# Kernel optimization log

Hardware: AMD Instinct MI355X
Metric: run time of the kernel (lower is better)

Reference implementation:

```python
import jax, jax.numpy as jnp
import numpy as np

B_ROWS = 262144
D = 64            # features
N_UNMASKED = D // 2
HID = 128
N_BINS = 8
BOUND = 3.0
MIN_BIN_W = 1e-3
MIN_BIN_H = 1e-3
MIN_DERIV = 1e-3
LN_EPS = 1e-6


def setup_inputs() -> dict:
    key = jax.random.key(0)
    ks = jax.random.split(key, 8)
    x = jax.random.normal(ks[0], (B_ROWS, D), dtype=jnp.float32)
    # conditioner MLP params (lecun-normal-ish)
    W0 = jax.random.normal(ks[1], (N_UNMASKED, HID), dtype=jnp.float32) / np.sqrt(N_UNMASKED)
    b0 = jnp.zeros((HID,), jnp.float32)
    g0 = jnp.ones((HID,), jnp.float32)
    be0 = jnp.zeros((HID,), jnp.float32)
    W1 = jax.random.normal(ks[2], (HID, HID), dtype=jnp.float32) / np.sqrt(HID)
    b1 = jnp.zeros((HID,), jnp.float32)
    g1 = jnp.ones((HID,), jnp.float32)
    be1 = jnp.zeros((HID,), jnp.float32)
    # spline output projection: HID -> N_UNMASKED * (3*K + 1)
    n_out = N_UNMASKED * (3 * N_BINS + 1)
    Wp = jax.random.normal(ks[3], (HID, n_out), dtype=jnp.float32) / np.sqrt(HID)
    bp = jnp.zeros((n_out,), jnp.float32)
    return {"x": x, "W0": W0, "b0": b0, "g0": g0, "be0": be0,
            "W1": W1, "b1": b1, "g1": g1, "be1": be1, "Wp": Wp, "bp": bp}


def _layer_norm(h, scale, bias):
    mu = jnp.mean(h, axis=-1, keepdims=True)
    var = jnp.mean(jnp.square(h - mu), axis=-1, keepdims=True)
    return (h - mu) * jax.lax.rsqrt(var + LN_EPS) * scale + bias


def _rqs_forward(xu, widths, heights, derivs):
    """Monotone rational-quadratic spline (Durkan et al. 2019), forward.
    xu: (..., D2); widths/heights: (..., D2, K); derivs: (..., D2, K+1)."""
    K = widths.shape[-1]
    cw = jnp.concatenate([jnp.zeros_like(widths[..., :1]), jnp.cumsum(widths, -1)], -1) - BOUND
    ch = jnp.concatenate([jnp.zeros_like(heights[..., :1]), jnp.cumsum(heights, -1)], -1) - BOUND
    inside = (xu > -BOUND) & (xu < BOUND)
    xc = jnp.clip(xu, -BOUND, BOUND)
    # bin search: index of bin containing xc
    idx = jnp.clip(jnp.sum(xc[..., None] >= cw, axis=-1) - 1, 0, K - 1)
    g = lambda t, i: jnp.take_along_axis(t, i[..., None], axis=-1)[..., 0]
    w_k = g(widths, idx); x_k = g(cw, idx)
    h_k = g(heights, idx); y_k = g(ch, idx)
    d_k = g(derivs, idx); d_k1 = g(derivs, idx + 1)
    s = h_k / w_k                       # bin slope
    theta = (xc - x_k) / w_k
    t1m = theta * (1.0 - theta)
    den = s + (d_k1 + d_k - 2.0 * s) * t1m
    y_in = y_k + h_k * (s * theta * theta + d_k * t1m) / den
    ld_in = (2.0 * jnp.log(s)
             + jnp.log(d_k1 * theta * theta + 2.0 * s * t1m + d_k * (1.0 - theta) ** 2)
             - 2.0 * jnp.log(den))
    y = jnp.where(inside, y_in, xu)           # identity outside domain
    ld = jnp.where(inside, ld_in, 0.0)
    return y, jnp.sum(ld, axis=-1)


def _forward(x, W0, b0, g0, be0, W1, b1, g1, be1, Wp, bp):
    # split by mask parity 0: even idx masked, odd idx transformed
    xm = x[..., 0::2]
    xu = x[..., 1::2]
    # conditioner MLP (LayerNorm + relu, residual when widths match)
    h1 = jax.nn.relu(_layer_norm(xm @ W0 + b0, g0, be0))
    h2 = jax.nn.relu(_layer_norm(h1 @ W1 + b1, g1, be1)) + h1  # residual (128==128)
    raw = (h2 @ Wp + bp).reshape(x.shape[:-1] + (N_UNMASKED, 3 * N_BINS + 1))
    # unconstrained -> rqs params
    w_raw = raw[..., :N_BINS]
    h_raw = raw[..., N_BINS:2 * N_BINS]
    d_raw = raw[..., 2 * N_BINS:]
    widths = jax.nn.softmax(w_raw, axis=-1)
    widths = (MIN_BIN_W + (1.0 - MIN_BIN_W * N_BINS) * widths) * (2.0 * BOUND)
    heights = jax.nn.softmax(h_raw, axis=-1)
    heights = (MIN_BIN_H + (1.0 - MIN_BIN_H * N_BINS) * heights) * (2.0 * BOUND)
    derivs = jax.nn.softplus(d_raw) + MIN_DERIV
    yu, log_det = _rqs_forward(xu, widths, heights, derivs)
    # merge by mask
    y = jnp.zeros_like(x)
    y = y.at[..., 0::2].set(xm)
    y = y.at[..., 1::2].set(yu)
    return y, log_det


def reference(x, W0, b0, g0, be0, W1, b1, g1, be1, Wp, bp):
    return _forward(x, W0, b0, g0, be0, W1, b1, g1, be1, Wp, bp)
```

## Files before the change

kernel.cpp:

```cpp
#include <hip/hip_runtime.h>
#include <hip/hip_bf16.h>
#include <stdint.h>

#define NROWS 262144

typedef __bf16 bf16x8 __attribute__((ext_vector_type(8)));
typedef float f32x4 __attribute__((ext_vector_type(4)));
typedef float f32x16 __attribute__((ext_vector_type(16)));

#define MFMA16(a,b,c) __builtin_amdgcn_mfma_f32_16x16x32_bf16(a,b,c,0,0,0)
#define MFMA32(a,b,c) __builtin_amdgcn_mfma_f32_32x32x16_bf16(a,b,c,0,0,0)

#define WS_WP 0
#define WS_W1 524288
#define WS_W0 589824
#define WS_BP 606208

#define RS0 0
#define RS1 16384
#define XMA 32768
#define W0L 40960
#define YUL 32768
#define LDL 49152
#define XUL 57344

__device__ __forceinline__ unsigned short f2bf(float f){
    unsigned int u = __float_as_uint(f);
    u = (u + 0x7FFFu + ((u >> 16) & 1u)) >> 16;
    return (unsigned short)u;
}
__device__ __forceinline__ float bf2f(unsigned short h){
    return __uint_as_float(((unsigned int)h) << 16);
}

__global__ __launch_bounds__(256) void prep_kernel(
    const float* __restrict__ W0, const float* __restrict__ W1,
    const float* __restrict__ Wp, const float* __restrict__ bp,
    char* __restrict__ ws)
{
    int tid = blockIdx.x * 256 + threadIdx.x;
    if (tid < 32768){
        int d = tid >> 10, r = tid & 1023;
        int plane = r >> 9, oct = (r >> 5) & 15, p = r & 31;
        unsigned short cell[8];
        #pragma unroll
        for (int j = 0; j < 8; j++){
            int k = oct*8 + j;
            float v = (p < 25) ? Wp[k*800 + d*25 + p] : 0.f;
            unsigned short hi = f2bf(v);
            cell[j] = plane ? f2bf(v - bf2f(hi)) : hi;
        }
        *(uint4*)(ws + WS_WP + d*16384 + plane*8192 + oct*512 + p*16) = *(uint4*)cell;
    } else if (tid < 36864){
        int i = tid - 32768;
        int kr = i >> 10, r = i & 1023;
        int plane = r >> 9, q = (r >> 7) & 3, n = r & 127;
        unsigned short cell[8];
        #pragma unroll
        for (int j = 0; j < 8; j++){
            int k = kr*32 + q*8 + j;
            float v = W1[k*128 + n];
            unsigned short hi = f2bf(v);
            cell[j] = plane ? f2bf(v - bf2f(hi)) : hi;
        }
        *(uint4*)(ws + WS_W1 + kr*16384 + plane*8192 + (q*128+n)*16) = *(uint4*)cell;
    } else if (tid < 37888){
        int i = tid - 36864;
        int plane = i >> 9, g = (i >> 7) & 3, n = i & 127;
        unsigned short cell[8];
        #pragma unroll
        for (int j = 0; j < 8; j++){
            int k = g*8 + j;
            float v = W0[k*128 + n];
            unsigned short hi = f2bf(v);
            cell[j] = plane ? f2bf(v - bf2f(hi)) : hi;
        }
        *(uint4*)(ws + WS_W0 + plane*8192 + (g*128+n)*16) = *(uint4*)cell;
    } else if (tid < 38912){
        int i = tid - 37888;
        int d = i >> 5, n = i & 31;
        ((float*)(ws + WS_BP))[i] = (n < 25) ? bp[d*25 + n] : 0.f;
    }
}

__global__ __launch_bounds__(256, 2) void main_kernel(
    const float* __restrict__ x,
    const float* __restrict__ pb0, const float* __restrict__ pg0, const float* __restrict__ pbe0,
    const float* __restrict__ pb1, const float* __restrict__ pg1, const float* __restrict__ pbe1,
    const char* __restrict__ ws,
    float* __restrict__ yout, float* __restrict__ ldout)
{
    __shared__ __align__(16) char smem[65536];
    const int t = threadIdx.x;
    const int r0 = blockIdx.x * 64;
    const int w = t >> 6, lane = t & 63, l16 = lane & 15, q = lane >> 4;
    const f32x4 fzero = {0.f, 0.f, 0.f, 0.f};

    auto stage16k = [&](int dstoff, int srcoff){
        #pragma unroll
        for (int k = 0; k < 4; k++){
            int cell = t + 256*k;
            ((uint4*)(smem + dstoff))[cell] = ((const uint4*)(ws + srcoff))[cell];
        }
    };

    #pragma unroll
    for (int k = 0; k < 4; k++){
        int i = t + 256*k;
        int row = i >> 4, s = i & 15;
        float4 v = ((const float4*)(x + (size_t)(r0 + row) * 64))[s];
        unsigned short h0 = f2bf(v.x), h1s = f2bf(v.z);
        unsigned short l0 = f2bf(v.x - bf2f(h0)), l1 = f2bf(v.z - bf2f(h1s));
        int g = s >> 2, ofs = (s & 3) * 4;
        *(unsigned int*)(smem + XMA + (g*64 + row)*16 + ofs) = (unsigned int)h0 | ((unsigned int)h1s << 16);
        *(unsigned int*)(smem + XMA + 4096 + (g*64 + row)*16 + ofs) = (unsigned int)l0 | ((unsigned int)l1 << 16);
        *(float*)(smem + XUL + ((2*s)*64 + row)*4) = v.y;
        *(float*)(smem + XUL + ((2*s+1)*64 + row)*4) = v.w;
    }
    stage16k(W0L, WS_W0);
    stage16k(RS0, WS_W1);
    __syncthreads();

    float h1r[8][4];
    {
        bf16x8 a_h = *(const bf16x8*)(smem + XMA + (q*64 + 16*w + l16)*16);
        bf16x8 a_l = *(const bf16x8*)(smem + XMA + 4096 + (q*64 + 16*w + l16)*16);
        f32x4 c0[8];
        #pragma unroll
        for (int nt = 0; nt < 8; nt++){
            int n = nt*16 + l16;
            bf16x8 b_h = *(const bf16x8*)(smem + W0L + (q*128 + n)*16);
            bf16x8 b_l = *(const bf16x8*)(smem + W0L + 8192 + (q*128 + n)*16);
            f32x4 acc = fzero;
            acc = MFMA16(a_h, b_l, acc);
            acc = MFMA16(a_l, b_h, acc);
            acc = MFMA16(a_h, b_h, acc);
            c0[nt] = acc;
        }
        float s1[4] = {0,0,0,0}, s2[4] = {0,0,0,0};
        #pragma unroll
        for (int nt = 0; nt < 8; nt++){
            float bv = pb0[nt*16 + l16];
            #pragma unroll
            for (int rg = 0; rg < 4; rg++){
                float v = c0[nt][rg] + bv;
                c0[nt][rg] = v; s1[rg] += v; s2[rg] += v*v;
            }
        }
        #pragma unroll
        for (int m = 1; m < 16; m <<= 1)
            #pragma unroll
            for (int rg = 0; rg < 4; rg++){
                s1[rg] += __shfl_xor(s1[rg], m, 64);
                s2[rg] += __shfl_xor(s2[rg], m, 64);
            }
        #pragma unroll
        for (int rg = 0; rg < 4; rg++){
            float mean = s1[rg] * 0.0078125f;
            float var  = s2[rg] * 0.0078125f - mean*mean;
            s1[rg] = mean; s2[rg] = rsqrtf(var + 1e-6f);
        }
        #pragma unroll
        for (int nt = 0; nt < 8; nt++){
            float gv = pg0[nt*16 + l16], bev = pbe0[nt*16 + l16];
            #pragma unroll
            for (int rg = 0; rg < 4; rg++){
                float hv = (c0[nt][rg] - s1[rg]) * s2[rg] * gv + bev;
                h1r[nt][rg] = fmaxf(hv, 0.f);
            }
        }
    }
    __syncthreads();

    stage16k(RS1, WS_W1 + 16384);
    bf16x8 ah1[4], al1[4];
    {
        char* sb = smem + 32768 + w*4096;
        #pragma unroll
        for (int nt = 0; nt < 8; nt++){
            int col = nt*16 + l16;
            #pragma unroll
            for (int rg = 0; rg < 4; rg++)
                *(unsigned short*)(sb + ((col>>3)*16 + q*4+rg)*16 + (col&7)*2) = f2bf(h1r[nt][rg]);
        }
        #pragma unroll
        for (int kr = 0; kr < 4; kr++)
            ah1[kr] = *(const bf16x8*)(sb + ((kr*4+q)*16 + l16)*16);
        #pragma unroll
        for (int nt = 0; nt < 8; nt++){
            int col = nt*16 + l16;
            #pragma unroll
            for (int rg = 0; rg < 4; rg++){
                unsigned short hi = f2bf(h1r[nt][rg]);
                *(unsigned short*)(sb + ((col>>3)*16 + q*4+rg)*16 + (col&7)*2) = f2bf(h1r[nt][rg] - bf2f(hi));
            }
        }
        #pragma unroll
        for (int kr = 0; kr < 4; kr++)
            al1[kr] = *(const bf16x8*)(sb + ((kr*4+q)*16 + l16)*16);
    }

    f32x4 c1[8];
    #pragma unroll
    for (int nt = 0; nt < 8; nt++) c1[nt] = fzero;
    auto g1round = [&](int base, bf16x8 ah, bf16x8 al){
        #pragma unroll
        for (int nt = 0; nt < 8; nt++){
            int n = nt*16 + l16;
            bf16x8 bhv = *(const bf16x8*)(smem + base + (q*128 + n)*16);
            bf16x8 blv = *(const bf16x8*)(smem + base + 8192 + (q*128 + n)*16);
            c1[nt] = MFMA16(ah, blv, c1[nt]);
            c1[nt] = MFMA16(al, bhv, c1[nt]);
            c1[nt] = MFMA16(ah, bhv, c1[nt]);
        }
    };
    g1round(RS0, ah1[0], al1[0]);
    __syncthreads();
    stage16k(RS0, WS_W1 + 32768);
    g1round(RS1, ah1[1], al1[1]);
    __syncthreads();
    stage16k(RS1, WS_W1 + 49152);
    g1round(RS0, ah1[2], al1[2]);
    __syncthreads();
    g1round(RS1, ah1[3], al1[3]);

    {
        float s1[4] = {0,0,0,0}, s2[4] = {0,0,0,0};
        #pragma unroll
        for (int nt = 0; nt < 8; nt++){
            float bv = pb1[nt*16 + l16];
            #pragma unroll
            for (int rg = 0; rg < 4; rg++){
                float v = c1[nt][rg] + bv;
                c1[nt][rg] = v; s1[rg] += v; s2[rg] += v*v;
            }
        }
        #pragma unroll
        for (int m = 1; m < 16; m <<= 1)
            #pragma unroll
            for (int rg = 0; rg < 4; rg++){
                s1[rg] += __shfl_xor(s1[rg], m, 64);
                s2[rg] += __shfl_xor(s2[rg], m, 64);
            }
        #pragma unroll
        for (int rg = 0; rg < 4; rg++){
            float mean = s1[rg] * 0.0078125f;
            float var  = s2[rg] * 0.0078125f - mean*mean;
            s1[rg] = mean; s2[rg] = rsqrtf(var + 1e-6f);
        }
        #pragma unroll
        for (int nt = 0; nt < 8; nt++){
            float gv = pg1[nt*16 + l16], bev = pbe1[nt*16 + l16];
            #pragma unroll
            for (int rg = 0; rg < 4; rg++){
                float hv = (c1[nt][rg] - s1[rg]) * s2[rg] * gv + bev;
                h1r[nt][rg] = fmaxf(hv, 0.f) + h1r[nt][rg];
            }
        }
    }
    __syncthreads();

    #pragma unroll
    for (int nt = 0; nt < 8; nt++){
        int k = nt*16 + l16;
        #pragma unroll
        for (int rg = 0; rg < 4; rg++){
            int row = 16*w + q*4 + rg;
            float val = h1r[nt][rg];
            unsigned short hi = f2bf(val);
            int addr = row*256 + ((((k>>3) ^ (row&15)) & 15)*16) + (k&7)*2;
            *(unsigned short*)(smem + RS0 + addr) = hi;
            *(unsigned short*)(smem + RS1 + addr) = f2bf(val - bf2f(hi));
        }
    }
    __syncthreads();
    bf16x8 bh[2][8], bl[2][8];
    #pragma unroll
    for (int T = 0; T < 2; T++)
        #pragma unroll
        for (int kb = 0; kb < 8; kb++){
            int r = T*32 + (lane & 31);
            int oct = kb*2 + (lane >> 5);
            int addr = r*256 + (((oct ^ (r&15)) & 15)*16);
            bh[T][kb] = *(const bf16x8*)(smem + RS0 + addr);
            bl[T][kb] = *(const bf16x8*)(smem + RS1 + addr);
        }

    const char* wpl = ws + WS_WP + lane*16;
    const float* bpf = (const float*)(ws + WS_BP);
    float* xuLf = (float*)(smem + XUL);
    float* yuLf = (float*)(smem + YUL);
    const uint4 zero4 = {0,0,0,0};
    const bool pok = (lane & 31) < 25;
    const int hh = lane >> 5;
    const int d0 = w*8;
    uint4 A0[8], A1[8];
    #pragma unroll
    for (int kk = 0; kk < 8; kk++){ A0[kk] = zero4; A1[kk] = zero4; }
    if (pok){
        #pragma unroll
        for (int kk = 0; kk < 4; kk++){
            A0[kk]   = *(const uint4*)(wpl + d0*16384 + kk*1024);
            A0[4+kk] = *(const uint4*)(wpl + d0*16384 + 8192 + kk*1024);
        }
    }
    float ld_acc = 0.f;
    for (int i = 0; i < 8; i++){
        int c = d0 + i;
        if (pok){
            #pragma unroll
            for (int kk = 0; kk < 4; kk++){
                A1[kk]   = *(const uint4*)(wpl + c*16384 + (4+kk)*1024);
                A1[4+kk] = *(const uint4*)(wpl + c*16384 + 8192 + (4+kk)*1024);
            }
        }
        f32x16 t0, t1;
        #pragma unroll
        for (int z = 0; z < 16; z++){ t0[z] = 0.f; t1[z] = 0.f; }
        #pragma unroll
        for (int kk = 0; kk < 4; kk++){
            bf16x8 ahh = *(bf16x8*)&A0[kk];
            bf16x8 all = *(bf16x8*)&A0[4+kk];
            t0 = MFMA32(ahh, bl[0][kk], t0); t1 = MFMA32(ahh, bl[1][kk], t1);
            t0 = MFMA32(all, bh[0][kk], t0); t1 = MFMA32(all, bh[1][kk], t1);
            t0 = MFMA32(ahh, bh[0][kk], t0); t1 = MFMA32(ahh, bh[1][kk], t1);
        }
        if (i < 7 && pok){
            #pragma unroll
            for (int kk = 0; kk < 4; kk++){
                A0[kk]   = *(const uint4*)(wpl + (c+1)*16384 + kk*1024);
                A0[4+kk] = *(const uint4*)(wpl + (c+1)*16384 + 8192 + kk*1024);
            }
        }
        #pragma unroll
        for (int kk = 0; kk < 4; kk++){
            bf16x8 ahh = *(bf16x8*)&A1[kk];
            bf16x8 all = *(bf16x8*)&A1[4+kk];
            t0 = MFMA32(ahh, bl[0][4+kk], t0); t1 = MFMA32(ahh, bl[1][4+kk], t1);
            t0 = MFMA32(all, bh[0][4+kk], t0); t1 = MFMA32(all, bh[1][4+kk], t1);
            t0 = MFMA32(ahh, bh[0][4+kk], t0); t1 = MFMA32(ahh, bh[1][4+kk], t1);
        }
        float xu0 = xuLf[c*64 + (lane & 31)];
        float xu1 = xuLf[c*64 + 32 + (lane & 31)];
        float xc0 = fminf(fmaxf(xu0, -3.f), 3.f);
        float xc1 = fminf(fmaxf(xu1, -3.f), 3.f);
        float4 bq0 = *(const float4*)(bpf + c*32 + 0  + 4*hh);
        float4 bq1 = *(const float4*)(bpf + c*32 + 8  + 4*hh);
        float4 bq2 = *(const float4*)(bpf + c*32 + 16 + 4*hh);
        float  bq3 = bpf[c*32 + 24 + 4*hh];
        float wv0[4], wv1[4], hv0[4], hv1[4], dv0[4], dv1[4];
        #pragma unroll
        for (int jj = 0; jj < 4; jj++){
            wv0[jj] = t0[jj] + bq0[jj];  hv0[jj] = t0[4+jj] + bq1[jj];  dv0[jj] = t0[8+jj] + bq2[jj];
            wv1[jj] = t1[jj] + bq0[jj];  hv1[jj] = t1[4+jj] + bq1[jj];  dv1[jj] = t1[8+jj] + bq2[jj];
        }
        float dx0 = t0[12] + bq3, dx1 = t1[12] + bq3;
        float bd0 = __shfl_xor(hh ? dv0[0] : dx0, 32, 64);
        float bd1 = __shfl_xor(hh ? dv1[0] : dx1, 32, 64);
        auto softscale = [&](float* a){
            float m = fmaxf(fmaxf(a[0],a[1]), fmaxf(a[2],a[3]));
            m = fmaxf(m, __shfl_xor(m, 32, 64));
            float e0 = __expf(a[0]-m), e1 = __expf(a[1]-m), e2 = __expf(a[2]-m), e3 = __expf(a[3]-m);
            float s = (e0+e1)+(e2+e3);
            s += __shfl_xor(s, 32, 64);
            float sc = 5.952f / s;
            a[0] = fmaf(e0, sc, 0.006f); a[1] = fmaf(e1, sc, 0.006f);
            a[2] = fmaf(e2, sc, 0.006f); a[3] = fmaf(e3, sc, 0.006f);
        };
        softscale(wv0); softscale(hv0); softscale(wv1); softscale(hv1);
        auto candf = [&](float* wv, float* hv, float* dv, float bdr, float xc,
                         float& X, float& Y, float& W, float& H, float& DK, float& DK1, float& V){
            float pw0 = wv[0], pw1 = pw0+wv[1], pw2 = pw1+wv[2], pw3 = pw2+wv[3];
            float ph0 = hv[0], ph1 = ph0+hv[1], ph2 = ph1+hv[2], ph3 = ph2+hv[3];
            float offw = __shfl_xor(pw3, 32, 64);
            float offh = __shfl_xor(ph3, 32, 64);
            float bw = hh ? (offw - 3.f) : -3.f;
            float by = hh ? (offh - 3.f) : -3.f;
            X = bw; Y = by; W = wv[0]; H = hv[0]; DK = dv[0]; DK1 = dv[1];
            float e1_ = bw + pw0, e2_ = bw + pw1, e3_ = bw + pw2;
            if (xc >= e1_){ X = e1_; Y = by + ph0; W = wv[1]; H = hv[1]; DK = dv[1]; DK1 = dv[2]; }
            if (xc >= e2_){ X = e2_; Y = by + ph1; W = wv[2]; H = hv[2]; DK = dv[2]; DK1 = dv[3]; }
            if (xc >= e3_){ X = e3_; Y = by + ph2; W = wv[3]; H = hv[3]; DK = dv[3]; DK1 = bdr;  }
            V = (!hh || xc >= bw) ? 1.f : 0.f;
        };
        float X0,Y0,Wc0,Hc0,K0,K10,V0, X1,Y1,Wc1,Hc1,K1,K11,V1;
        candf(wv0, hv0, dv0, bd0, xc0, X0,Y0,Wc0,Hc0,K0,K10,V0);
        candf(wv1, hv1, dv1, bd1, xc1, X1,Y1,Wc1,Hc1,K1,K11,V1);
        float rX  = __shfl_xor(hh ? X0  : X1 , 32, 64);
        float rY  = __shfl_xor(hh ? Y0  : Y1 , 32, 64);
        float rW  = __shfl_xor(hh ? Wc0 : Wc1, 32, 64);
        float rH  = __shfl_xor(hh ? Hc0 : Hc1, 32, 64);
        float rK  = __shfl_xor(hh ? K0  : K1 , 32, 64);
        float rK1 = __shfl_xor(hh ? K10 : K11, 32, 64);
        float rV  = __shfl_xor(hh ? V0  : V1 , 32, 64);
        float oX  = hh ? X1  : X0,  oY  = hh ? Y1  : Y0,  oW = hh ? Wc1 : Wc0;
        float oH  = hh ? Hc1 : Hc0, oK  = hh ? K1  : K0,  oK1 = hh ? K11 : K10;
        float oV  = hh ? V1  : V0;
        bool useh1 = ((hh ? oV : rV) > 0.5f);
        bool useOwn = (hh != 0) == useh1;
        float X = useOwn ? oX : rX,  Y = useOwn ? oY : rY;
        float W = useOwn ? oW : rW,  H = useOwn ? oH : rH;
        float K = useOwn ? oK : rK,  K1s = useOwn ? oK1 : rK1;
        float xu = hh ? xu1 : xu0;
        float xc = hh ? xc1 : xc0;
        float DKs  = fmaxf(K, 0.f)   + __logf(1.f + __expf(-fabsf(K)))   + 0.001f;
        float DK1s = fmaxf(K1s, 0.f) + __logf(1.f + __expf(-fabsf(K1s))) + 0.001f;
        float iw = 1.f / W;
        float s_ = H * iw;
        float th = (xc - X) * iw;
        float om = 1.f - th;
        float t1m = th * om;
        float den = s_ + (DK1s + DKs - 2.f*s_) * t1m;
        float yin = Y + H * (s_*th*th + DKs*t1m) / den;
        float num2 = DK1s*th*th + 2.f*s_*t1m + DKs*om*om;
        float ldin = 2.f*__logf(s_) + __logf(num2) - 2.f*__logf(den);
        bool inside = (xu > -3.f) && (xu < 3.f);
        yuLf[c*64 + lane] = inside ? yin : xu;
        ld_acc += inside ? ldin : 0.f;
    }

    *(float*)(smem + LDL + (w*64 + lane)*4) = ld_acc;
    __syncthreads();
    if (t < 64){
        const float* lp = (const float*)(smem + LDL);
        ldout[r0 + t] = (lp[t] + lp[64 + t]) + (lp[128 + t] + lp[192 + t]);
    }
    {
        int row = t >> 2, part = t & 3;
        const float* xrow = x + (size_t)(r0 + row)*64;
        float* yrow = yout + (size_t)(r0 + row)*64;
        const float* yuL = (const float*)(smem + YUL);
        #pragma unroll
        for (int j = 0; j < 4; j++){
            int s = part*4 + j;
            float4 xv = ((const float4*)xrow)[s];
            float4 o;
            o.x = xv.x; o.z = xv.z;
            o.y = yuL[(2*s)*64 + row];
            o.w = yuL[(2*s+1)*64 + row];
            ((float4*)yrow)[s] = o;
        }
    }
}

extern "C" void kernel_launch(void* const* d_in, const int* in_sizes, int n_in,
                              void* d_out, int out_size, void* d_ws, size_t ws_size,
                              hipStream_t stream)
{
    const float* x   = (const float*)d_in[0];
    const float* W0  = (const float*)d_in[1];
    const float* b0  = (const float*)d_in[2];
    const float* g0  = (const float*)d_in[3];
    const float* be0 = (const float*)d_in[4];
    const float* W1  = (const float*)d_in[5];
    const float* b1  = (const float*)d_in[6];
    const float* g1  = (const float*)d_in[7];
    const float* be1 = (const float*)d_in[8];
    const float* Wp  = (const float*)d_in[9];
    const float* bp  = (const float*)d_in[10];
    float* y = (float*)d_out;
    float* ldo = y + (size_t)NROWS * 64;
    char* ws = (char*)d_ws;

    hipLaunchKernelGGL(prep_kernel, dim3(152), dim3(256), 0, stream, W0, W1, Wp, bp, ws);
    hipLaunchKernelGGL(main_kernel, dim3(4096), dim3(256), 0, stream,
                       x, b0, g0, be0, b1, g1, be1, ws, y, ldo);
}
```

Baseline: 410.5 us.

## Shrink LDS footprint to fit three blocks per CU

Reduces shared memory from 64 KB to 48 KB by loading W0 fragments directly into registers, staging W1 in two 16 KB halves, and reusing buffers for the yu/log-det outputs, then raises launch bounds to 3 blocks per SM. The projection B fragments are now read from LDS inside the loop instead of being held in 32 register vectors, freeing registers for the higher occupancy target. It costs extra LDS reads per chunk in the projection loop and an extra barrier, and the register cap at 3 waves/SIMD may cause spills.

```diff
diff --git a/kernel.cpp b/kernel.cpp
--- a/kernel.cpp
+++ b/kernel.cpp
@@ -16,13 +16,10 @@
 #define WS_W0 589824
 #define WS_BP 606208
 
-#define RS0 0
-#define RS1 16384
-#define XMA 32768
-#define W0L 40960
-#define YUL 32768
-#define LDL 49152
-#define XUL 57344
+#define W1A 0
+#define W1B 16384
+#define XM  32768
+#define XU  40960
 
 __device__ __forceinline__ unsigned short f2bf(float f){
     unsigned int u = __float_as_uint(f);
@@ -83,14 +80,14 @@
     }
 }
 
-__global__ __launch_bounds__(256, 2) void main_kernel(
+__global__ __launch_bounds__(256, 3) void main_kernel(
     const float* __restrict__ x,
     const float* __restrict__ pb0, const float* __restrict__ pg0, const float* __restrict__ pbe0,
     const float* __restrict__ pb1, const float* __restrict__ pg1, const float* __restrict__ pbe1,
     const char* __restrict__ ws,
     float* __restrict__ yout, float* __restrict__ ldout)
 {
-    __shared__ __align__(16) char smem[65536];
+    __shared__ __align__(16) char smem[49152];
     const int t = threadIdx.x;
     const int r0 = blockIdx.x * 64;
     const int w = t >> 6, lane = t & 63, l16 = lane & 15, q = lane >> 4;
@@ -104,6 +101,13 @@
         }
     };
 
+    uint4 w0h[8], w0l[8];
+    #pragma unroll
+    for (int nt = 0; nt < 8; nt++){
+        int n = nt*16 + l16;
+        w0h[nt] = *(const uint4*)(ws + WS_W0 + (q*128 + n)*16);
+        w0l[nt] = *(const uint4*)(ws + WS_W0 + 8192 + (q*128 + n)*16);
+    }
     #pragma unroll
     for (int k = 0; k < 4; k++){
         int i = t + 256*k;
@@ -112,25 +116,24 @@
         unsigned short h0 = f2bf(v.x), h1s = f2bf(v.z);
         unsigned short l0 = f2bf(v.x - bf2f(h0)), l1 = f2bf(v.z - bf2f(h1s));
         int g = s >> 2, ofs = (s & 3) * 4;
-        *(unsigned int*)(smem + XMA + (g*64 + row)*16 + ofs) = (unsigned int)h0 | ((unsigned int)h1s << 16);
-        *(unsigned int*)(smem + XMA + 4096 + (g*64 + row)*16 + ofs) = (unsigned int)l0 | ((unsigned int)l1 << 16);
-        *(float*)(smem + XUL + ((2*s)*64 + row)*4) = v.y;
-        *(float*)(smem + XUL + ((2*s+1)*64 + row)*4) = v.w;
-    }
-    stage16k(W0L, WS_W0);
-    stage16k(RS0, WS_W1);
+        *(unsigned int*)(smem + XM + (g*64 + row)*16 + ofs) = (unsigned int)h0 | ((unsigned int)h1s << 16);
+        *(unsigned int*)(smem + XM + 4096 + (g*64 + row)*16 + ofs) = (unsigned int)l0 | ((unsigned int)l1 << 16);
+        *(float*)(smem + XU + ((2*s)*64 + row)*4) = v.y;
+        *(float*)(smem + XU + ((2*s+1)*64 + row)*4) = v.w;
+    }
+    stage16k(W1A, WS_W1);
+    stage16k(W1B, WS_W1 + 16384);
     __syncthreads();
 
     float h1r[8][4];
     {
-        bf16x8 a_h = *(const bf16x8*)(smem + XMA + (q*64 + 16*w + l16)*16);
-        bf16x8 a_l = *(const bf16x8*)(smem + XMA + 4096 + (q*64 + 16*w + l16)*16);
+        bf16x8 a_h = *(const bf16x8*)(smem + XM + (q*64 + 16*w + l16)*16);
+        bf16x8 a_l = *(const bf16x8*)(smem + XM + 4096 + (q*64 + 16*w + l16)*16);
         f32x4 c0[8];
         #pragma unroll
         for (int nt = 0; nt < 8; nt++){
-            int n = nt*16 + l16;
-            bf16x8 b_h = *(const bf16x8*)(smem + W0L + (q*128 + n)*16);
-            bf16x8 b_l = *(const bf16x8*)(smem + W0L + 8192 + (q*128 + n)*16);
+            bf16x8 b_h = *(bf16x8*)&w0h[nt];
+            bf16x8 b_l = *(bf16x8*)&w0l[nt];
             f32x4 acc = fzero;
             acc = MFMA16(a_h, b_l, acc);
             acc = MFMA16(a_l, b_h, acc);
@@ -172,32 +175,39 @@
     }
     __syncthreads();
 
-    stage16k(RS1, WS_W1 + 16384);
     bf16x8 ah1[4], al1[4];
     {
-        char* sb = smem + 32768 + w*4096;
-        #pragma unroll
-        for (int nt = 0; nt < 8; nt++){
-            int col = nt*16 + l16;
-            #pragma unroll
-            for (int rg = 0; rg < 4; rg++)
-                *(unsigned short*)(sb + ((col>>3)*16 + q*4+rg)*16 + (col&7)*2) = f2bf(h1r[nt][rg]);
-        }
-        #pragma unroll
-        for (int kr = 0; kr < 4; kr++)
-            ah1[kr] = *(const bf16x8*)(sb + ((kr*4+q)*16 + l16)*16);
-        #pragma unroll
-        for (int nt = 0; nt < 8; nt++){
-            int col = nt*16 + l16;
-            #pragma unroll
-            for (int rg = 0; rg < 4; rg++){
-                unsigned short hi = f2bf(h1r[nt][rg]);
-                *(unsigned short*)(sb + ((col>>3)*16 + q*4+rg)*16 + (col&7)*2) = f2bf(h1r[nt][rg] - bf2f(hi));
-            }
-        }
-        #pragma unroll
-        for (int kr = 0; kr < 4; kr++)
-            al1[kr] = *(const bf16x8*)(sb + ((kr*4+q)*16 + l16)*16);
+        char* sb = smem + XM + w*2048;
+        #pragma unroll
+        for (int half = 0; half < 2; half++){
+            #pragma unroll
+            for (int nt = half*4; nt < half*4 + 4; nt++){
+                int col = nt*16 + l16;
+                int gg = (col >> 3) - half*8;
+                #pragma unroll
+                for (int rg = 0; rg < 4; rg++)
+                    *(unsigned short*)(sb + (gg*16 + q*4+rg)*16 + (col&7)*2) = f2bf(h1r[nt][rg]);
+            }
+            #pragma unroll
+            for (int kr = half*2; kr < half*2 + 2; kr++)
+                ah1[kr] = *(const bf16x8*)(sb + (((kr*4+q) - half*8)*16 + l16)*16);
+        }
+        #pragma unroll
+        for (int half = 0; half < 2; half++){
+            #pragma unroll
+            for (int nt = half*4; nt < half*4 + 4; nt++){
+                int col = nt*16 + l16;
+                int gg = (col >> 3) - half*8;
+                #pragma unroll
+                for (int rg = 0; rg < 4; rg++){
+                    unsigned short hi = f2bf(h1r[nt][rg]);
+                    *(unsigned short*)(sb + (gg*16 + q*4+rg)*16 + (col&7)*2) = f2bf(h1r[nt][rg] - bf2f(hi));
+                }
+            }
+            #pragma unroll
+            for (int kr = half*2; kr < half*2 + 2; kr++)
+                al1[kr] = *(const bf16x8*)(sb + (((kr*4+q) - half*8)*16 + l16)*16);
+        }
     }
 
     f32x4 c1[8];
@@ -214,15 +224,14 @@
             c1[nt] = MFMA16(ah, bhv, c1[nt]);
         }
     };
-    g1round(RS0, ah1[0], al1[0]);
-    __syncthreads();
-    stage16k(RS0, WS_W1 + 32768);
-    g1round(RS1, ah1[1], al1[1]);
-    __syncthreads();
-    stage16k(RS1, WS_W1 + 49152);
-    g1round(RS0, ah1[2], al1[2]);
-    __syncthreads();
-    g1round(RS1, ah1[3], al1[3]);
+    g1round(W1A, ah1[0], al1[0]);
+    g1round(W1B, ah1[1], al1[1]);
+    __syncthreads();
+    stage16k(W1A, WS_W1 + 32768);
+    stage16k(W1B, WS_W1 + 49152);
+    __syncthreads();
+    g1round(W1A, ah1[2], al1[2]);
+    g1round(W1B, ah1[3], al1[3]);
 
     {
         float s1[4] = {0,0,0,0}, s2[4] = {0,0,0,0};
@@ -269,31 +278,24 @@
             float val = h1r[nt][rg];
             unsigned short hi = f2bf(val);
             int addr = row*256 + ((((k>>3) ^ (row&15)) & 15)*16) + (k&7)*2;
-            *(unsigned short*)(smem + RS0 + addr) = hi;
-            *(unsigned short*)(smem + RS1 + addr) = f2bf(val - bf2f(hi));
-        }
-    }
-    __syncthreads();
-    bf16x8 bh[2][8], bl[2][8];
-    #pragma unroll
-    for (int T = 0; T < 2; T++)
-        #pragma unroll
-        for (int kb = 0; kb < 8; kb++){
-            int r = T*32 + (lane & 31);
-            int oct = kb*2 + (lane >> 5);
-            int addr = r*256 + (((oct ^ (r&15)) & 15)*16);
-            bh[T][kb] = *(const bf16x8*)(smem + RS0 + addr);
-            bl[T][kb] = *(const bf16x8*)(smem + RS1 + addr);
-        }
+            *(unsigned short*)(smem + W1A + addr) = hi;
+            *(unsigned short*)(smem + W1B + addr) = f2bf(val - bf2f(hi));
+        }
+    }
+    __syncthreads();
 
     const char* wpl = ws + WS_WP + lane*16;
     const float* bpf = (const float*)(ws + WS_BP);
-    float* xuLf = (float*)(smem + XUL);
-    float* yuLf = (float*)(smem + YUL);
+    float* xuLf = (float*)(smem + XU);
+    float* yuLf = (float*)(smem + XM);
     const uint4 zero4 = {0,0,0,0};
     const bool pok = (lane & 31) < 25;
     const int hh = lane >> 5;
     const int d0 = w*8;
+    const int rA = (lane & 31)*256, rB = (32 + (lane & 31))*256;
+    auto rdB = [&](int pl, int rbase, int oct){
+        return *(const bf16x8*)(smem + pl + rbase + (((oct ^ l16) & 15)*16));
+    };
     uint4 A0[8], A1[8];
     #pragma unroll
     for (int kk = 0; kk < 8; kk++){ A0[kk] = zero4; A1[kk] = zero4; }
@@ -319,11 +321,14 @@
         for (int z = 0; z < 16; z++){ t0[z] = 0.f; t1[z] = 0.f; }
         #pragma unroll
         for (int kk = 0; kk < 4; kk++){
+            int oct = kk*2 + hh;
             bf16x8 ahh = *(bf16x8*)&A0[kk];
             bf16x8 all = *(bf16x8*)&A0[4+kk];
-            t0 = MFMA32(ahh, bl[0][kk], t0); t1 = MFMA32(ahh, bl[1][kk], t1);
-            t0 = MFMA32(all, bh[0][kk], t0); t1 = MFMA32(all, bh[1][kk], t1);
-            t0 = MFMA32(ahh, bh[0][kk], t0); t1 = MFMA32(ahh, bh[1][kk], t1);
+            bf16x8 b0h = rdB(W1A, rA, oct), b0l = rdB(W1B, rA, oct);
+            bf16x8 b1h = rdB(W1A, rB, oct), b1l = rdB(W1B, rB, oct);
+            t0 = MFMA32(ahh, b0l, t0); t1 = MFMA32(ahh, b1l, t1);
+            t0 = MFMA32(all, b0h, t0); t1 = MFMA32(all, b1h, t1);
+            t0 = MFMA32(ahh, b0h, t0); t1 = MFMA32(ahh, b1h, t1);
         }
         if (i < 7 && pok){
             #pragma unroll
@@ -334,11 +339,14 @@
         }
         #pragma unroll
         for (int kk = 0; kk < 4; kk++){
+            int oct = (4+kk)*2 + hh;
             bf16x8 ahh = *(bf16x8*)&A1[kk];
             bf16x8 all = *(bf16x8*)&A1[4+kk];
-            t0 = MFMA32(ahh, bl[0][4+kk], t0); t1 = MFMA32(ahh, bl[1][4+kk], t1);
-            t0 = MFMA32(all, bh[0][4+kk], t0); t1 = MFMA32(all, bh[1][4+kk], t1);
-            t0 = MFMA32(ahh, bh[0][4+kk], t0); t1 = MFMA32(ahh, bh[1][4+kk], t1);
+            bf16x8 b0h = rdB(W1A, rA, oct), b0l = rdB(W1B, rA, oct);
+            bf16x8 b1h = rdB(W1A, rB, oct), b1l = rdB(W1B, rB, oct);
+            t0 = MFMA32(ahh, b0l, t0); t1 = MFMA32(ahh, b1l, t1);
+            t0 = MFMA32(all, b0h, t0); t1 = MFMA32(all, b1h, t1);
+            t0 = MFMA32(ahh, b0h, t0); t1 = MFMA32(ahh, b1h, t1);
         }
         float xu0 = xuLf[c*64 + (lane & 31)];
         float xu1 = xuLf[c*64 + 32 + (lane & 31)];
@@ -419,17 +427,18 @@
         ld_acc += inside ? ldin : 0.f;
     }
 
-    *(float*)(smem + LDL + (w*64 + lane)*4) = ld_acc;
+    __syncthreads();
+    *(float*)(smem + XU + (w*64 + lane)*4) = ld_acc;
     __syncthreads();
     if (t < 64){
-        const float* lp = (const float*)(smem + LDL);
+        const float* lp = (const float*)(smem + XU);
         ldout[r0 + t] = (lp[t] + lp[64 + t]) + (lp[128 + t] + lp[192 + t]);
     }
     {
         int row = t >> 2, part = t & 3;
         const float* xrow = x + (size_t)(r0 + row)*64;
         float* yrow = yout + (size_t)(r0 + row)*64;
-        const float* yuL = (const float*)(smem + YUL);
+        const float* yuL = (const float*)(smem + XM);
         #pragma unroll
         for (int j = 0; j < 4; j++){
             int s = part*4 + j;
```

Result: faster. 389.7 us (-5.1%).
